# Kernel tuning notes

Hardware: AMD Instinct MI355X
Metric: run time of the kernel (lower is better)

## Reference

```python
import jax, jax.numpy as jnp
import numpy as np

B, N, L, C = 4, 16, 192, 64
H = 128
ROW, COL = 16, 12  # L == ROW*COL, ROW >= COL
NUM = 2  # class_num


def setup_inputs() -> dict:
    key = jax.random.key(0)
    ks = jax.random.split(key, 12)
    s = 1.0 / np.sqrt(H).astype(np.float32)
    u = lambda k, shape: jax.random.uniform(k, shape, jnp.float32, -s, s)
    return {
        "x": jax.random.normal(ks[0], (B, N, L, C), jnp.float32),
        "pad_mask": jnp.ones((B, N), jnp.bool_),
        "fc3_w": u(ks[1], (H, C)), "fc3_b": u(ks[2], (H,)),
        "fc4_w": u(ks[3], (H, H)), "fc4_b": u(ks[4], (H,)),
        "W_enc": u(ks[5], (NUM, 6 * H, 3 * H)), "B_enc": u(ks[6], (NUM, 6 * H)),
        "fc1_w": u(ks[7], (NUM, 1, H)), "fc1_b": u(ks[8], (NUM, 1)),
        "fc2_w": u(ks[9], (NUM, 1, H)), "fc2_b": u(ks[10], (NUM, 1)),
    }


def _witran_encoder(a, W, Bb):
    # a: [COL*BN, slice_len, H] diagonally-shifted input; W: [6H, 3H]; Bb: [6H]
    RBN, slice_len, _ = a.shape
    BN = RBN // COL
    R = COL  # Water2sea_slice_num (after permute(2,0,1,3), slices run over col)
    slice_ids = jnp.arange(RBN) // BN
    xs = jnp.transpose(a, (1, 0, 2))  # [slice_len, RBN, H]

    def step(carry, inp):
        h_row, h_col = carry
        x_s, s = inp
        g = jnp.concatenate([h_row, h_col, x_s], axis=-1) @ W.T  # [RBN, 6H]
        # torch adds bias only to first batch*(s+1) rows, and only while s < slice_num
        mask = (slice_ids <= s) & (s < R)
        g = g + jnp.where(mask[:, None], Bb, jnp.zeros((), g.dtype))
        sig = jax.nn.sigmoid(g[:, : 4 * H])
        th = jnp.tanh(g[:, 4 * H:])
        u_r, o_r, u_c, o_c = jnp.split(sig, 4, axis=-1)
        i_r, i_c = jnp.split(th, 2, axis=-1)
        h_row = jnp.tanh((1 - u_r) * h_row + u_r * i_r) * o_r
        h_col = jnp.tanh((1 - u_c) * h_col + u_c * i_c) * o_c
        # saved pieces (only valid for late s; we keep the last, which is always valid)
        loc = jnp.clip(s - ROW + 1, 0, R - 1)
        row_save = jax.lax.dynamic_slice_in_dim(h_row, loc * BN, BN, axis=0)
        col_save = h_col[(R - 1) * BN:, :]  # save BEFORE roll, as in torch
        h_col = jnp.roll(h_col, BN, axis=0)
        return (h_row, h_col), (row_save, col_save)

    h0 = jnp.zeros((RBN, H), a.dtype)
    (_, _), (row_saves, col_saves) = jax.lax.scan(
        step, (h0, h0), (xs, jnp.arange(slice_len)))
    # last entries == hidden_row_all[:, -1, -1, :], hidden_col_all[:, -1, -1, :]
    return row_saves[-1], col_saves[-1]  # each [BN, H]


def reference(x, pad_mask, fc3_w, fc3_b, fc4_w, fc4_b, W_enc, B_enc,
              fc1_w, fc1_b, fc2_w, fc2_b):
    Bn, Nn = x.shape[0], x.shape[1]
    h = jax.nn.relu(x @ fc3_w.T + fc3_b) @ fc4_w.T + fc4_b  # [B,N,L,H]
    xr = h.reshape(-1, ROW, COL, H)          # [BN, row, col, H]
    inp = jnp.transpose(xr, (2, 0, 1, 3))    # [col, BN, row, H]
    slice_len = COL + ROW - 1
    # diagonal 'water2sea' shift: transfer[r, :, r:r+ROW] = inp[r]
    padded = jnp.pad(inp, ((0, 0), (0, 0), (0, COL - 1), (0, 0)))
    transfer = jax.vmap(lambda t, r: jnp.roll(t, r, axis=1))(padded, jnp.arange(COL))
    a = transfer.reshape(COL * Bn * Nn, slice_len, H)

    def per_class(W, Bb, f1w, f1b, f2w, f2b):
        row_last, col_last = _witran_encoder(a, W, Bb)
        # torch: row := hidden_col_all tail, col := hidden_row_all tail
        out = 0.5 * (col_last @ f1w.T + f1b) + 0.5 * (row_last @ f2w.T + f2b)
        return out[:, 0]  # [BN]

    y = jax.vmap(per_class)(W_enc, B_enc, fc1_w, fc1_b, fc2_w, fc2_b)  # [NUM, BN]
    return jnp.transpose(y).reshape(Bn, Nn, NUM)
```

## Files before the change

### kernel.cpp

```cpp
#include <hip/hip_runtime.h>

typedef _Float16 hf;
typedef _Float16 half2v __attribute__((ext_vector_type(2)));
typedef _Float16 half8 __attribute__((ext_vector_type(8)));
typedef float f32x4 __attribute__((ext_vector_type(4)));
typedef int int4v __attribute__((ext_vector_type(4)));

constexpr int Steps = 27;

constexpr int OFF_WX = 393216;
constexpr int OFF_F3 = 589824;
constexpr int OFF_F4 = 598016;
constexpr int OFF_XW = 614400;
constexpr int CST = 136;

__device__ __forceinline__ int aidx(int r, int k) {
  int blk = k >> 3;
  return r * 256 + (((blk ^ (r & 7)) & 31) << 3) + (k & 7);
}
__device__ __forceinline__ int hidx(int r, int k) {
  int blk = k >> 3;
  return r * 128 + (((blk ^ (r & 15)) & 15) << 3) + (k & 7);
}
__device__ __forceinline__ int xidx(int r, int k) {
  int blk = k >> 3;
  return r * 64 + (((blk ^ (r & 7)) & 7) << 3) + (k & 7);
}
__device__ __forceinline__ float sigmoidf_(float x) { return 1.0f / (1.0f + __expf(-x)); }
__device__ __forceinline__ float tanh_(float x) { return 1.0f - 2.0f / (__expf(2.0f * x) + 1.0f); }

__global__ __launch_bounds__(512) void prep(const float* __restrict__ fc3_w,
                                            const float* __restrict__ fc4_w,
                                            const float* __restrict__ W_enc,
                                            hf* __restrict__ wsh) {
  int idx = blockIdx.x * 512 + threadIdx.x;
  if (idx >= OFF_XW) return;
  float v;
  if (idx < OFF_WX) {
    int jj = idx & 7, lane = (idx >> 3) & 63, rest = idx >> 9;
    int ks = rest & 7; rest >>= 3;
    int j = rest % 3; rest /= 3;
    int wv = rest & 15, cls = rest >> 4;
    int gate = (wv < 8) ? (j < 2 ? j : 4) : (j < 2 ? j + 2 : 5);
    int n = gate * 128 + (wv & 7) * 16 + (lane & 15);
    int k = ks * 32 + ((lane >> 4) << 3) + jj;
    v = W_enc[(cls * 768 + n) * 384 + k];
  } else if (idx < OFF_F3) {
    int f = idx - OFF_WX;
    int j = f & 7, lane = (f >> 3) & 63, rest = f >> 9;
    int ks = rest & 3; rest >>= 2;
    int wv = rest & 7; rest >>= 3;
    int gate = rest % 6, cls = rest / 6;
    int n = gate * 128 + wv * 16 + (lane & 15);
    int k = 256 + ks * 32 + ((lane >> 4) << 3) + j;
    v = W_enc[(cls * 768 + n) * 384 + k];
  } else if (idx < OFF_F4) {
    int f = idx - OFF_F3;
    int j = f & 7, lane = (f >> 3) & 63, rest = f >> 9;
    int ks = rest & 1, wv = rest >> 1;
    int n = wv * 16 + (lane & 15), k = ks * 32 + ((lane >> 4) << 3) + j;
    v = fc3_w[n * 64 + k];
  } else {
    int f = idx - OFF_F4;
    int j = f & 7, lane = (f >> 3) & 63, rest = f >> 9;
    int ks = rest & 3, wv = rest >> 2;
    int n = wv * 16 + (lane & 15), k = ks * 32 + ((lane >> 4) << 3) + j;
    v = fc4_w[n * 128 + k];
  }
  wsh[idx] = (hf)v;
}

__global__ __launch_bounds__(512) void prelude(
    const float* __restrict__ x, const float* __restrict__ fc3_b, const float* __restrict__ fc4_b,
    const float* __restrict__ B_enc, const hf* __restrict__ wsh, hf* __restrict__ xWb) {
  const int t = threadIdx.x, lane = t & 63, wv = t >> 6;
  const int c16 = lane & 15, quad = lane >> 4;
  const int row0 = blockIdx.x * 64, bn = row0 / 192, l0 = row0 % 192;
  const int d = wv * 16 + c16;

  __shared__ __attribute__((aligned(16))) hf xA[64 * 64];
  __shared__ __attribute__((aligned(16))) hf hbuf[64 * 128];
  __shared__ __attribute__((aligned(16))) hf xout[64 * 768];
  __shared__ float actf[64];

  {
    int r = t >> 3, cb = (t & 7) * 8;
    const float* xp = x + (size_t)(row0 + r) * 64 + cb;
    f32x4 a = *(const f32x4*)xp, b = *(const f32x4*)(xp + 4);
    half8 h;
    h[0] = (hf)a.x; h[1] = (hf)a.y; h[2] = (hf)a.z; h[3] = (hf)a.w;
    h[4] = (hf)b.x; h[5] = (hf)b.y; h[6] = (hf)b.z; h[7] = (hf)b.w;
    *(half8*)&xA[xidx(r, cb)] = h;
  }
  if (t < 64) {
    int l = l0 + t;
    actf[t] = ((l / 12) + (l % 12)) < 12 ? 1.f : 0.f;
  }
  __syncthreads();

  {
    float b3v = fc3_b[d];
    half8 w0 = *(const half8*)(wsh + OFF_F3 + (wv * 2 + 0) * 512 + lane * 8);
    half8 w1 = *(const half8*)(wsh + OFF_F3 + (wv * 2 + 1) * 512 + lane * 8);
    f32x4 acc[4] = {{0, 0, 0, 0}, {0, 0, 0, 0}, {0, 0, 0, 0}, {0, 0, 0, 0}};
#pragma unroll
    for (int mt = 0; mt < 4; ++mt) {
      half8 a0 = *(const half8*)&xA[xidx(mt * 16 + c16, quad * 8)];
      half8 a1 = *(const half8*)&xA[xidx(mt * 16 + c16, 32 + quad * 8)];
      acc[mt] = __builtin_amdgcn_mfma_f32_16x16x32_f16(a0, w0, acc[mt], 0, 0, 0);
      acc[mt] = __builtin_amdgcn_mfma_f32_16x16x32_f16(a1, w1, acc[mt], 0, 0, 0);
    }
#pragma unroll
    for (int mt = 0; mt < 4; ++mt)
#pragma unroll
      for (int r = 0; r < 4; ++r)
        hbuf[hidx(mt * 16 + quad * 4 + r, d)] = (hf)fmaxf(acc[mt][r] + b3v, 0.f);
  }
  __syncthreads();

  {
    float b4v = fc4_b[d];
    half8 w4[4];
#pragma unroll
    for (int ks = 0; ks < 4; ++ks)
      w4[ks] = *(const half8*)(wsh + OFF_F4 + (wv * 4 + ks) * 512 + lane * 8);
    f32x4 acc[4] = {{0, 0, 0, 0}, {0, 0, 0, 0}, {0, 0, 0, 0}, {0, 0, 0, 0}};
#pragma unroll
    for (int mt = 0; mt < 4; ++mt)
#pragma unroll
      for (int ks = 0; ks < 4; ++ks) {
        half8 a = *(const half8*)&hbuf[hidx(mt * 16 + c16, ks * 32 + quad * 8)];
        acc[mt] = __builtin_amdgcn_mfma_f32_16x16x32_f16(a, w4[ks], acc[mt], 0, 0, 0);
      }
    __syncthreads();
#pragma unroll
    for (int mt = 0; mt < 4; ++mt)
#pragma unroll
      for (int r = 0; r < 4; ++r)
        hbuf[hidx(mt * 16 + quad * 4 + r, d)] = (hf)(acc[mt][r] + b4v);
  }
  __syncthreads();

  half8 af[4][4];
#pragma unroll
  for (int mt = 0; mt < 4; ++mt)
#pragma unroll
    for (int ks = 0; ks < 4; ++ks)
      af[mt][ks] = *(const half8*)&hbuf[hidx(mt * 16 + c16, ks * 32 + quad * 8)];

  for (int cls = 0; cls < 2; ++cls) {
    for (int g = 0; g < 6; ++g) {
      int pos = (g < 2) ? g : (g < 4 ? g + 1 : (g == 4 ? 2 : 5));
      half8 wf[4];
#pragma unroll
      for (int ks = 0; ks < 4; ++ks)
        wf[ks] = *(const half8*)(wsh + OFF_WX + (((cls * 6 + g) * 8 + wv) * 4 + ks) * 512 + lane * 8);
      float bv = B_enc[cls * 768 + g * 128 + d];
#pragma unroll
      for (int mt = 0; mt < 4; ++mt) {
        f32x4 acc = {0.f, 0.f, 0.f, 0.f};
#pragma unroll
        for (int ks = 0; ks < 4; ++ks)
          acc = __builtin_amdgcn_mfma_f32_16x16x32_f16(af[mt][ks], wf[ks], acc, 0, 0, 0);
#pragma unroll
        for (int r = 0; r < 4; ++r) {
          int row = mt * 16 + quad * 4 + r;
          xout[row * 768 + d * 6 + pos] = (hf)(acc[r] + actf[row] * bv);
        }
      }
    }
    __syncthreads();
    {
      const int* src = (const int*)xout;
      int* dst = (int*)(xWb + (((size_t)cls * 64 + bn) * 192 + l0) * 768);
#pragma unroll
      for (int i = 0; i < 12; ++i) {
        int base = (t + i * 512) * 4;
        *(int4v*)&dst[base] = *(const int4v*)&src[base];
      }
    }
    __syncthreads();
  }
}

__device__ __forceinline__ void xpre(const hf* __restrict__ xg, int t, int sN,
                                     unsigned* pa, unsigned* pb) {
#pragma unroll
  for (int i = 0; i < 3; ++i) {
    int u = t + (i << 10);
    int colf = u >= 1536;
    int q = colf ? u - 1536 : u;
    int c = q >> 7, dd = q & 127;
    int rr = sN - c;
    unsigned a = 0, b = 0;
    if (rr >= 0 && rr < 16) {
      const hf* p = xg + (size_t)(rr * 12 + c) * 768 + dd * 6;
      if (colf) {
        a = (unsigned)*(const unsigned short*)(p + 3);
        b = *(const unsigned*)(p + 4);
      } else {
        a = *(const unsigned*)p;
        b = (unsigned)*(const unsigned short*)(p + 2);
      }
    }
    pa[i] = a;
    pb[i] = b;
  }
}
__device__ __forceinline__ float lo16f(unsigned v) {
  return (float)__builtin_bit_cast(half2v, v)[0];
}
__device__ __forceinline__ float hi16f(unsigned v) {
  return (float)__builtin_bit_cast(half2v, v)[1];
}

__global__ __launch_bounds__(1024) __attribute__((amdgpu_waves_per_eu(4, 4))) void witran(
    const hf* __restrict__ wsh, const float* __restrict__ fc1_w, const float* __restrict__ fc1_b,
    const float* __restrict__ fc2_w, const float* __restrict__ fc2_b,
    const hf* __restrict__ xWb, float* __restrict__ out) {
  const int cls = blockIdx.x & 1, bn = blockIdx.x >> 1;
  const int t = threadIdx.x, lane = t & 63, wv = t >> 6;
  const int c16 = lane & 15, quad = lane >> 4;
  const int d = (wv & 7) * 16 + c16;
  const int goff = (wv < 8) ? 0 : 3;

  __shared__ __attribute__((aligned(16))) hf wlds[16 * 4096];
  __shared__ __attribute__((aligned(16))) hf A[4096];
  __shared__ hf g16[6 * 12 * CST];
  __shared__ float red[128];

  for (int i = t; i < 2048; i += 1024) ((int*)A)[i] = 0;

  half8 wr[2][8];
  {
    const hf* wb = wsh + (((size_t)(cls * 16 + wv) * 3) * 8) * 512 + lane * 8;
#pragma unroll
    for (int ks = 0; ks < 8; ++ks) {
      wr[0][ks] = *(const half8*)(wb + ks * 512);
      wr[1][ks] = *(const half8*)(wb + (8 + ks) * 512);
    }
#pragma unroll
    for (int f = 0; f < 8; ++f)
      *(half8*)&wlds[wv * 4096 + f * 512 + lane * 8] = *(const half8*)(wb + (16 + f) * 512);
  }

  const hf* xg = xWb + ((size_t)cls * 64 + bn) * 192 * 768;

  unsigned pa[3], pb[3];
  xpre(xg, t, 0, pa, pb);
  __syncthreads();

  for (int s = 0; s < Steps; ++s) {
    f32x4 a0 = {0, 0, 0, 0}, a1 = a0, a2 = a0;
#pragma unroll
    for (int ks = 0; ks < 8; ++ks) {
      half8 av = *(const half8*)&A[aidx(c16, ks * 32 + quad * 8)];
      a0 = __builtin_amdgcn_mfma_f32_16x16x32_f16(av, wr[0][ks], a0, 0, 0, 0);
      a1 = __builtin_amdgcn_mfma_f32_16x16x32_f16(av, wr[1][ks], a1, 0, 0, 0);
      half8 w2 = *(const half8*)&wlds[wv * 4096 + ks * 512 + lane * 8];
      a2 = __builtin_amdgcn_mfma_f32_16x16x32_f16(av, w2, a2, 0, 0, 0);
    }
    if (quad < 3) {
#pragma unroll
      for (int r = 0; r < 4; ++r) {
        int base = (quad * 4 + r) * CST + d;
        g16[(goff + 0) * 12 * CST + base] = (hf)a0[r];
        g16[(goff + 1) * 12 * CST + base] = (hf)a1[r];
        g16[(goff + 2) * 12 * CST + base] = (hf)a2[r];
      }
    }
    float hold[3];
#pragma unroll
    for (int i = 0; i < 3; ++i) {
      int u = t + (i << 10);
      int colf = u >= 1536;
      int q = colf ? u - 1536 : u;
      int c = q >> 7, dd = q & 127;
      hold[i] = (float)A[aidx(c, colf ? 128 + dd : dd)];
    }
    __syncthreads();

#pragma unroll
    for (int i = 0; i < 3; ++i) {
      int u = t + (i << 10);
      int colf = u >= 1536;
      int q = colf ? u - 1536 : u;
      int c = q >> 7, dd = q & 127;
      if (c <= s) {
        int base = c * CST + dd;
        int po = colf ? 3 : 0;
        float gu = (float)g16[(po + 0) * 12 * CST + base];
        float go = (float)g16[(po + 1) * 12 * CST + base];
        float gi = (float)g16[(po + 2) * 12 * CST + base];
        float xu, xo, xi;
        if (colf) {
          xu = lo16f(pa[i]); xo = lo16f(pb[i]); xi = hi16f(pb[i]);
        } else {
          xu = lo16f(pa[i]); xo = hi16f(pa[i]); xi = lo16f(pb[i]);
        }
        float uu = sigmoidf_(gu + xu), oo = sigmoidf_(go + xo), ii = tanh_(gi + xi);
        float h = tanh_((1.f - uu) * hold[i] + uu * ii) * oo;
        if (colf) {
          int c2 = (c == 11) ? 0 : c + 1;
          A[aidx(c2, 128 + dd)] = (hf)h;
        } else {
          A[aidx(c, dd)] = (hf)h;
        }
      }
    }
    xpre(xg, t, s + 1, pa, pb);
    __syncthreads();
  }

  if (t < 128) {
    float hr = (float)A[aidx(11, t)];
    float hc = (float)A[aidx(0, 128 + t)];
    red[t] = 0.5f * (hc * fc1_w[cls * 128 + t] + hr * fc2_w[cls * 128 + t]);
  }
  __syncthreads();
  if (t == 0) {
    float sum = 0.f;
    for (int i = 0; i < 128; ++i) sum += red[i];
    out[bn * 2 + cls] = sum + 0.5f * (fc1_b[cls] + fc2_b[cls]);
  }
}

extern "C" void kernel_launch(void* const* d_in, const int* in_sizes, int n_in,
                              void* d_out, int out_size, void* d_ws, size_t ws_size,
                              hipStream_t stream) {
  const float* x = (const float*)d_in[0];
  const float* fc3_w = (const float*)d_in[2];
  const float* fc3_b = (const float*)d_in[3];
  const float* fc4_w = (const float*)d_in[4];
  const float* fc4_b = (const float*)d_in[5];
  const float* W_enc = (const float*)d_in[6];
  const float* B_enc = (const float*)d_in[7];
  const float* fc1_w = (const float*)d_in[8];
  const float* fc1_b = (const float*)d_in[9];
  const float* fc2_w = (const float*)d_in[10];
  const float* fc2_b = (const float*)d_in[11];
  float* out = (float*)d_out;

  hf* wsh = (hf*)d_ws;
  hf* xWb = wsh + OFF_XW;

  prep<<<dim3(1200), dim3(512), 0, stream>>>(fc3_w, fc4_w, W_enc, wsh);
  prelude<<<dim3(192), dim3(512), 0, stream>>>(x, fc3_b, fc4_b, B_enc, wsh, xWb);
  witran<<<dim3(128), dim3(1024), 0, stream>>>(wsh, fc1_w, fc1_b, fc2_w, fc2_b, xWb, out);
}
```

Measured before the change: 187.2 us.

## Apply gates directly from MFMA accumulators with double-buffered hidden state

Each lane now applies the gate nonlinearity to its own MFMA accumulator outputs instead of writing the gate values to a shared g16 buffer and re-reading them after a barrier. The hidden state is ping-ponged between two LDS buffers, so one barrier per recurrence step replaces two. The x-projection loads are remapped to match the accumulator layout, and a custom barrier waits only on lgkmcnt. The aim is to remove LDS round-trips and a sync on the serial 27-step critical path. The trade-off is more LDS for the second hidden-state buffer and an updated-step mask that differs from the old c<=s check.

```diff
diff --git a/kernel.cpp b/kernel.cpp
--- a/kernel.cpp
+++ b/kernel.cpp
@@ -12,7 +12,6 @@
 constexpr int OFF_F3 = 589824;
 constexpr int OFF_F4 = 598016;
 constexpr int OFF_XW = 614400;
-constexpr int CST = 136;
 
 __device__ __forceinline__ int aidx(int r, int k) {
   int blk = k >> 3;
@@ -28,6 +27,14 @@
 }
 __device__ __forceinline__ float sigmoidf_(float x) { return 1.0f / (1.0f + __expf(-x)); }
 __device__ __forceinline__ float tanh_(float x) { return 1.0f - 2.0f / (__expf(2.0f * x) + 1.0f); }
+
+__device__ __forceinline__ void bar_lgkm() {
+  __builtin_amdgcn_sched_barrier(0);
+  asm volatile("s_waitcnt lgkmcnt(0)" ::: "memory");
+  __builtin_amdgcn_s_barrier();
+  __builtin_amdgcn_sched_barrier(0);
+  asm volatile("" ::: "memory");
+}
 
 __global__ __launch_bounds__(512) void prep(const float* __restrict__ fc3_w,
                                             const float* __restrict__ fc4_w,
@@ -183,19 +190,16 @@
   }
 }
 
-__device__ __forceinline__ void xpre(const hf* __restrict__ xg, int t, int sN,
-                                     unsigned* pa, unsigned* pb) {
-#pragma unroll
-  for (int i = 0; i < 3; ++i) {
-    int u = t + (i << 10);
-    int colf = u >= 1536;
-    int q = colf ? u - 1536 : u;
-    int c = q >> 7, dd = q & 127;
-    int rr = sN - c;
+__device__ __forceinline__ void xload4(const hf* __restrict__ pbase, int sN, int c0,
+                                       bool act, bool colw, unsigned* px, unsigned* py) {
+#pragma unroll
+  for (int r = 0; r < 4; ++r) {
+    int c = c0 + r;
+    unsigned rr = (unsigned)(sN - c);
     unsigned a = 0, b = 0;
-    if (rr >= 0 && rr < 16) {
-      const hf* p = xg + (size_t)(rr * 12 + c) * 768 + dd * 6;
-      if (colf) {
+    if (act && rr < 16u) {
+      const hf* p = pbase + (size_t)(rr * 12 + c) * 768;
+      if (colw) {
         a = (unsigned)*(const unsigned short*)(p + 3);
         b = *(const unsigned*)(p + 4);
       } else {
@@ -203,8 +207,8 @@
         b = (unsigned)*(const unsigned short*)(p + 2);
       }
     }
-    pa[i] = a;
-    pb[i] = b;
+    px[r] = a;
+    py[r] = b;
   }
 }
 __device__ __forceinline__ float lo16f(unsigned v) {
@@ -222,14 +226,16 @@
   const int t = threadIdx.x, lane = t & 63, wv = t >> 6;
   const int c16 = lane & 15, quad = lane >> 4;
   const int d = (wv & 7) * 16 + c16;
-  const int goff = (wv < 8) ? 0 : 3;
+  const bool colw = (wv >= 8);
+  const bool act = (quad < 3);
+  const int c0 = quad * 4;
+  const int kbase = colw ? 128 + d : d;
 
   __shared__ __attribute__((aligned(16))) hf wlds[16 * 4096];
-  __shared__ __attribute__((aligned(16))) hf A[4096];
-  __shared__ hf g16[6 * 12 * CST];
+  __shared__ __attribute__((aligned(16))) hf A[2][4096];
   __shared__ float red[128];
 
-  for (int i = t; i < 2048; i += 1024) ((int*)A)[i] = 0;
+  for (int i = t; i < 4096; i += 1024) ((int*)A)[i] = 0;
 
   half8 wr[2][8];
   {
@@ -244,77 +250,54 @@
       *(half8*)&wlds[wv * 4096 + f * 512 + lane * 8] = *(const half8*)(wb + (16 + f) * 512);
   }
 
-  const hf* xg = xWb + ((size_t)cls * 64 + bn) * 192 * 768;
-
-  unsigned pa[3], pb[3];
-  xpre(xg, t, 0, pa, pb);
-  __syncthreads();
+  const hf* xgd = xWb + ((size_t)cls * 64 + bn) * 192 * 768 + d * 6;
+
+  unsigned px[4], py[4];
+  xload4(xgd, 0, c0, act, colw, px, py);
+  bar_lgkm();
 
   for (int s = 0; s < Steps; ++s) {
+    const hf* __restrict__ Ac = A[s & 1];
+    hf* __restrict__ An = A[(s & 1) ^ 1];
+
     f32x4 a0 = {0, 0, 0, 0}, a1 = a0, a2 = a0;
 #pragma unroll
     for (int ks = 0; ks < 8; ++ks) {
-      half8 av = *(const half8*)&A[aidx(c16, ks * 32 + quad * 8)];
+      half8 av = *(const half8*)&Ac[aidx(c16, ks * 32 + quad * 8)];
       a0 = __builtin_amdgcn_mfma_f32_16x16x32_f16(av, wr[0][ks], a0, 0, 0, 0);
       a1 = __builtin_amdgcn_mfma_f32_16x16x32_f16(av, wr[1][ks], a1, 0, 0, 0);
       half8 w2 = *(const half8*)&wlds[wv * 4096 + ks * 512 + lane * 8];
       a2 = __builtin_amdgcn_mfma_f32_16x16x32_f16(av, w2, a2, 0, 0, 0);
     }
-    if (quad < 3) {
+
+    if (act) {
 #pragma unroll
       for (int r = 0; r < 4; ++r) {
-        int base = (quad * 4 + r) * CST + d;
-        g16[(goff + 0) * 12 * CST + base] = (hf)a0[r];
-        g16[(goff + 1) * 12 * CST + base] = (hf)a1[r];
-        g16[(goff + 2) * 12 * CST + base] = (hf)a2[r];
-      }
-    }
-    float hold[3];
-#pragma unroll
-    for (int i = 0; i < 3; ++i) {
-      int u = t + (i << 10);
-      int colf = u >= 1536;
-      int q = colf ? u - 1536 : u;
-      int c = q >> 7, dd = q & 127;
-      hold[i] = (float)A[aidx(c, colf ? 128 + dd : dd)];
-    }
-    __syncthreads();
-
-#pragma unroll
-    for (int i = 0; i < 3; ++i) {
-      int u = t + (i << 10);
-      int colf = u >= 1536;
-      int q = colf ? u - 1536 : u;
-      int c = q >> 7, dd = q & 127;
-      if (c <= s) {
-        int base = c * CST + dd;
-        int po = colf ? 3 : 0;
-        float gu = (float)g16[(po + 0) * 12 * CST + base];
-        float go = (float)g16[(po + 1) * 12 * CST + base];
-        float gi = (float)g16[(po + 2) * 12 * CST + base];
+        int c = c0 + r;
+        float hold = (float)Ac[aidx(c, kbase)];
         float xu, xo, xi;
-        if (colf) {
-          xu = lo16f(pa[i]); xo = lo16f(pb[i]); xi = hi16f(pb[i]);
+        if (colw) {
+          xu = lo16f(px[r]); xo = lo16f(py[r]); xi = hi16f(py[r]);
         } else {
-          xu = lo16f(pa[i]); xo = hi16f(pa[i]); xi = lo16f(pb[i]);
+          xu = lo16f(px[r]); xo = hi16f(px[r]); xi = lo16f(py[r]);
         }
-        float uu = sigmoidf_(gu + xu), oo = sigmoidf_(go + xo), ii = tanh_(gi + xi);
-        float h = tanh_((1.f - uu) * hold[i] + uu * ii) * oo;
-        if (colf) {
-          int c2 = (c == 11) ? 0 : c + 1;
-          A[aidx(c2, 128 + dd)] = (hf)h;
-        } else {
-          A[aidx(c, dd)] = (hf)h;
-        }
-      }
-    }
-    xpre(xg, t, s + 1, pa, pb);
-    __syncthreads();
-  }
-
+        float uu = sigmoidf_(a0[r] + xu);
+        float oo = sigmoidf_(a1[r] + xo);
+        float ii = tanh_(a2[r] + xi);
+        float h = tanh_(hold + uu * (ii - hold)) * oo;
+        int cw = colw ? (c == 11 ? 0 : c + 1) : c;
+        An[aidx(cw, kbase)] = (hf)h;
+      }
+    }
+
+    xload4(xgd, s + 1, c0, act, colw, px, py);
+    bar_lgkm();
+  }
+
+  const hf* Af = A[Steps & 1];
   if (t < 128) {
-    float hr = (float)A[aidx(11, t)];
-    float hc = (float)A[aidx(0, 128 + t)];
+    float hr = (float)Af[aidx(11, t)];
+    float hc = (float)Af[aidx(0, 128 + t)];
     red[t] = 0.5f * (hc * fc1_w[cls * 128 + t] + hr * fc2_w[cls * 128 + t]);
   }
   __syncthreads();
```

New measurement: 198.2 us. +5.9%, slower.
